# Optimization experiments

Measured on AMD Instinct MI355X. Metric: run time of the kernel, lower is better.

## Reference

```python
import jax, jax.numpy as jnp
from jax import lax
import numpy as np

VOCAB, EMB, UNITS, B, T = 32000, 256, 1024, 64, 128


def setup_inputs() -> dict:
    key = jax.random.key(0)
    k1, k2, k3, k4 = jax.random.split(key, 4)
    x = jax.random.randint(k1, (B, T), 0, VOCAB, dtype=jnp.int32)
    hidden = jnp.zeros((B, UNITS), jnp.float32)
    E = jax.random.normal(k2, (VOCAB, EMB), jnp.float32) * 0.05
    # Keras GRU kernel layout: columns = [z | r | h], each block of size UNITS
    W = jax.random.normal(k3, (EMB, 3 * UNITS), jnp.float32) * (1.0 / np.sqrt(EMB))
    U = jax.random.normal(k4, (UNITS, 3 * UNITS), jnp.float32) * (1.0 / np.sqrt(UNITS))
    b = jnp.zeros((2, 3 * UNITS), jnp.float32)  # [input_bias, recurrent_bias] (reset_after=True)
    return {"x": x, "hidden": hidden, "E": E, "W": W, "U": U, "b": b}


def reference(x, hidden, E, W, U, b):
    # Embedding lookup: [B, T, EMB]
    emb = E[x]
    # Precompute all input projections once (time-parallel GEMM): [B, T, 3*UNITS]
    xin = jnp.einsum('btd,dk->btk', emb, W) + b[0]

    def step(h, xt):
        # Recurrent projection with separate recurrent bias (reset_after=True)
        rec = h @ U + b[1]  # [B, 3*UNITS]
        xz, xr, xh = jnp.split(xt, 3, axis=-1)
        rz, rr, rh = jnp.split(rec, 3, axis=-1)
        z = jax.nn.sigmoid(xz + rz)
        r = jax.nn.sigmoid(xr + rr)
        hh = jnp.tanh(xh + r * rh)  # reset gate applied AFTER recurrent matmul
        h_new = z * h + (1.0 - z) * hh
        return h_new, h_new

    state, outs = lax.scan(step, hidden, jnp.swapaxes(xin, 0, 1))  # scan over T
    outputs = jnp.swapaxes(outs, 0, 1)  # [B, T, UNITS]
    return outputs, state
```

## Files before the change

kernel.cpp:

```cpp
#include <hip/hip_runtime.h>
#include <math.h>

typedef unsigned short u16;
typedef _Float16 f16;
typedef f16 v8h __attribute__((ext_vector_type(8)));
typedef float v4f __attribute__((ext_vector_type(4)));
typedef unsigned v4u __attribute__((ext_vector_type(4)));

union Frag { v8h h; u16 s[8]; unsigned u[4]; v4u u4; };
union HU { f16 h; u16 u; };

__device__ __forceinline__ void fsplit16s(float v, u16& hi, u16& lo) {
    HU a, b;
    float vs = v * 64.f;
    a.h = (f16)vs;
    float d = vs - (float)a.h;
    b.h = (f16)(d * 2048.f);
    hi = a.u; lo = b.u;
}

__device__ __forceinline__ void fsplit16d(double v, u16& hi, u16& lo) {
    HU a, b;
    double vs = v * 64.0;
    a.h = (f16)vs;
    float d = (float)(vs - (double)a.h);
    b.h = (f16)(d * 2048.f);
    hi = a.u; lo = b.u;
}

__device__ __forceinline__ void split8s(const float* __restrict__ p, v8h& hi, v8h& lo) {
    Frag h, l;
#pragma unroll
    for (int j = 0; j < 8; ++j) {
        u16 a, b;
        fsplit16s(p[j], a, b);
        h.s[j] = a;
        l.s[j] = b;
    }
    hi = h.h; lo = l.h;
}

__device__ __forceinline__ Frag load16_sc(const u16* p) {
    v4u r;
    asm volatile("global_load_dwordx4 %0, %1, off sc0 sc1" : "=v"(r) : "v"(p) : "memory");
    Frag f; f.u4 = r;
    return f;
}

__device__ __forceinline__ Frag load16_nc(const u16* p) {
    v4u r;
    asm volatile("global_load_dwordx4 %0, %1, off" : "=v"(r) : "v"(p) : "memory");
    Frag f; f.u4 = r;
    return f;
}

__global__ void prep_h(const float* __restrict__ hid, u16* __restrict__ hhi, u16* __restrict__ hlo) {
    int i = blockIdx.x * 256 + threadIdx.x;
    u16 h, l;
    fsplit16s(hid[i], h, l);
    hhi[i] = h;
    hlo[i] = l;
}

__global__ void transpose_split(const float* __restrict__ src, u16* __restrict__ dhi,
                                u16* __restrict__ dlo, int R, int C) {
    __shared__ float tile[32][33];
    int tid = threadIdx.x;
    int tx = tid & 31, ty = tid >> 5;
    int c0 = blockIdx.x * 32, r0 = blockIdx.y * 32;
#pragma unroll
    for (int i = 0; i < 4; ++i)
        tile[ty + i * 8][tx] = src[(size_t)(r0 + ty + i * 8) * C + c0 + tx];
    __syncthreads();
#pragma unroll
    for (int i = 0; i < 4; ++i) {
        int c = c0 + ty + i * 8;
        float v = tile[tx][ty + i * 8];
        size_t o = (size_t)c * R + r0 + tx;
        u16 h, l;
        fsplit16s(v, h, l);
        dhi[o] = h;
        dlo[o] = l;
    }
}

__global__ void init_barrier(unsigned* __restrict__ bar) {
    bar[blockIdx.x * 256 + threadIdx.x] = 0u;
}

__global__ __launch_bounds__(512, 1) void gru_persistent(
        const u16* __restrict__ UThi, const u16* __restrict__ UTlo,
        const u16* __restrict__ WThi, const u16* __restrict__ WTlo,
        const float* __restrict__ b, const int* __restrict__ x,
        const float* __restrict__ E, const float* __restrict__ hid,
        u16* __restrict__ hhi0, u16* __restrict__ hhi1,
        u16* __restrict__ hlo0, u16* __restrict__ hlo1,
        float* __restrict__ out, unsigned* __restrict__ bar) {
    __shared__ u16 u_lds[3 * 128 * 17 * 8];
    __shared__ float red[4][8][256];
    int tid = threadIdx.x;
    int w = tid >> 6, lane = tid & 63;
    int n = lane & 15, q = lane >> 4;
    int bg = blockIdx.x >> 6;
    int ut = blockIdx.x & 63;
    int b0r = bg * 16;
    int u0 = ut * 16;
    unsigned* sf = bar + bg * 256;
    unsigned* poll_addr = sf + w * 32 + (lane & 31);

    for (int i = tid; i < 3 * 128 * 16; i += 512) {
        int g = i >> 11;
        int rem = i & 2047;
        int chunk = rem >> 4;
        int col = rem & 15;
        *(v4u*)(u_lds + (size_t)((g * 128 + chunk) * 17 + col) * 8) =
            *(const v4u*)(UThi + (size_t)(g * 1024 + u0 + col) * 1024 + chunk * 8);
    }
    __syncthreads();

    size_t aoff = (size_t)(b0r + n) * 1024 + w * 128 + q * 8;
    size_t uloff = (size_t)(u0 + n) * 1024 + w * 128 + q * 8;

    Frag Wh_r[3], Wl_r[3];
#pragma unroll
    for (int g = 0; g < 3; ++g) {
        size_t wo = (size_t)(g * 1024 + u0 + n) * 256 + w * 32 + q * 8;
        Wh_r[g].u4 = *(const v4u*)(WThi + wo);
        Wl_r[g].u4 = *(const v4u*)(WTlo + wo);
    }

    const int* xrow = x + (size_t)(b0r + n) * 128;

    int bl = tid >> 4, ul = tid & 15;
    int bb = b0r + bl;
    int u = u0 + ul;
    size_t ho = (size_t)bb * 1024 + u;
    double bz = 0.0, br_ = 0.0, bxh = 0.0, brh = 0.0, hp = 0.0;
    if (tid < 256) {
        bz = (double)b[u0 + ul] + (double)b[3072 + u0 + ul];
        br_ = (double)b[1024 + u0 + ul] + (double)b[3072 + 1024 + u0 + ul];
        bxh = (double)b[2048 + u0 + ul];
        brh = (double)b[3072 + 2048 + u0 + ul];
        hp = (double)hid[ho];
    }

    const float S12 = 2.44140625e-4f;
    const float S23 = 1.1920928955078125e-7f;

    for (int t = 0; t < 128; ++t) {
        const u16* hhi_in = (t & 1) ? hhi1 : hhi0;
        const u16* hlo_in = (t & 1) ? hlo1 : hlo0;
        u16* hhi_out = (t & 1) ? hhi0 : hhi1;
        u16* hlo_out = (t & 1) ? hlo0 : hlo1;

        Frag Blo[3][4];
#pragma unroll
        for (int g = 0; g < 3; ++g)
#pragma unroll
            for (int kk = 0; kk < 4; ++kk)
                Blo[g][kk] = load16_nc(UTlo + uloff + (size_t)g * 1048576 + kk * 32);

        v4f az = {0.f, 0.f, 0.f, 0.f}, ag = az, ah = az;
        v4f azl = az, agl = az, ahl = az;
        v4f axh = az, axhl = az;

        {
            int tok = xrow[t];
            const float* erow = E + (size_t)tok * 256 + w * 32 + q * 8;
            v8h EAh, EAl;
            split8s(erow, EAh, EAl);
            az  = __builtin_amdgcn_mfma_f32_16x16x32_f16(EAh, Wh_r[0].h, az, 0, 0, 0);
            ag  = __builtin_amdgcn_mfma_f32_16x16x32_f16(EAh, Wh_r[1].h, ag, 0, 0, 0);
            axh = __builtin_amdgcn_mfma_f32_16x16x32_f16(EAh, Wh_r[2].h, axh, 0, 0, 0);
            azl  = __builtin_amdgcn_mfma_f32_16x16x32_f16(EAl, Wh_r[0].h, azl, 0, 0, 0);
            agl  = __builtin_amdgcn_mfma_f32_16x16x32_f16(EAl, Wh_r[1].h, agl, 0, 0, 0);
            axhl = __builtin_amdgcn_mfma_f32_16x16x32_f16(EAl, Wh_r[2].h, axhl, 0, 0, 0);
            azl  = __builtin_amdgcn_mfma_f32_16x16x32_f16(EAh, Wl_r[0].h, azl, 0, 0, 0);
            agl  = __builtin_amdgcn_mfma_f32_16x16x32_f16(EAh, Wl_r[1].h, agl, 0, 0, 0);
            axhl = __builtin_amdgcn_mfma_f32_16x16x32_f16(EAh, Wl_r[2].h, axhl, 0, 0, 0);
        }

        if (t > 0) {
            unsigned target = (unsigned)t;
            while (true) {
                unsigned v = __hip_atomic_load(poll_addr, __ATOMIC_RELAXED, __HIP_MEMORY_SCOPE_AGENT);
                if (__all(v >= target)) break;
                __builtin_amdgcn_s_sleep(1);
            }
        }

        v8h Ah[4], Al[4];
#pragma unroll
        for (int kk = 0; kk < 4; ++kk) {
            Ah[kk] = load16_sc(hhi_in + aoff + kk * 32).h;
            Al[kk] = load16_sc(hlo_in + aoff + kk * 32).h;
        }
        asm volatile("s_waitcnt vmcnt(0)" ::: "memory");

#pragma unroll
        for (int kk = 0; kk < 4; ++kk) {
            int chunk = w * 16 + kk * 4 + q;
            const u16* lp = u_lds + (size_t)(chunk * 17 + n) * 8;
            Frag f0, f1, f2;
            f0.u4 = *(const v4u*)(lp);
            f1.u4 = *(const v4u*)(lp + 128 * 17 * 8);
            f2.u4 = *(const v4u*)(lp + 2 * 128 * 17 * 8);
            v8h Bh0 = f0.h, Bh1 = f1.h, Bh2 = f2.h;
            az = __builtin_amdgcn_mfma_f32_16x16x32_f16(Ah[kk], Bh0, az, 0, 0, 0);
            ag = __builtin_amdgcn_mfma_f32_16x16x32_f16(Ah[kk], Bh1, ag, 0, 0, 0);
            ah = __builtin_amdgcn_mfma_f32_16x16x32_f16(Ah[kk], Bh2, ah, 0, 0, 0);
            azl = __builtin_amdgcn_mfma_f32_16x16x32_f16(Al[kk], Bh0, azl, 0, 0, 0);
            agl = __builtin_amdgcn_mfma_f32_16x16x32_f16(Al[kk], Bh1, agl, 0, 0, 0);
            ahl = __builtin_amdgcn_mfma_f32_16x16x32_f16(Al[kk], Bh2, ahl, 0, 0, 0);
            azl = __builtin_amdgcn_mfma_f32_16x16x32_f16(Ah[kk], Blo[0][kk].h, azl, 0, 0, 0);
            agl = __builtin_amdgcn_mfma_f32_16x16x32_f16(Ah[kk], Blo[1][kk].h, agl, 0, 0, 0);
            ahl = __builtin_amdgcn_mfma_f32_16x16x32_f16(Ah[kk], Blo[2][kk].h, ahl, 0, 0, 0);
        }

        __syncthreads();
#pragma unroll
        for (int r = 0; r < 4; ++r) {
            int idx = (q * 4 + r) * 16 + n;
            red[0][w][idx] = az[r] * S12 + azl[r] * S23;
            red[1][w][idx] = ag[r] * S12 + agl[r] * S23;
            red[2][w][idx] = ah[r] * S12 + ahl[r] * S23;
            red[3][w][idx] = axh[r] * S12 + axhl[r] * S23;
        }
        __syncthreads();

        if (tid < 256) {
            double rz = bz, rr = br_, rh = brh, xh = bxh;
#pragma unroll
            for (int ww = 0; ww < 8; ++ww) {
                rz += (double)red[0][ww][tid];
                rr += (double)red[1][ww][tid];
                rh += (double)red[2][ww][tid];
                xh += (double)red[3][ww][tid];
            }
            size_t bt = (size_t)bb * 128 + t;
            double z = 1.0 / (1.0 + exp(-rz));
            double rg = 1.0 / (1.0 + exp(-rr));
            double hh = tanh(xh + rg * rh);
            double hn = z * hp + (1.0 - z) * hh;
            hp = hn;
            float hnf = (float)hn;

            if (t < 127) {
                u16 myhi, mylo;
                fsplit16d(hn, myhi, mylo);
                unsigned me = (unsigned)myhi | ((unsigned)mylo << 16);
                unsigned ot = __shfl_xor(me, 1);
                if ((tid & 1) == 0) {
                    unsigned hi32 = (me & 0xFFFFu) | ((ot & 0xFFFFu) << 16);
                    unsigned lo32 = (me >> 16) | (ot & 0xFFFF0000u);
                    __hip_atomic_store((unsigned*)(hhi_out + ho), hi32, __ATOMIC_RELAXED, __HIP_MEMORY_SCOPE_AGENT);
                    __hip_atomic_store((unsigned*)(hlo_out + ho), lo32, __ATOMIC_RELAXED, __HIP_MEMORY_SCOPE_AGENT);
                }
                asm volatile("s_waitcnt vmcnt(0)" ::: "memory");
                if (lane == 0)
                    __hip_atomic_store(sf + ut * 4 + w, (unsigned)(t + 1),
                                       __ATOMIC_RELAXED, __HIP_MEMORY_SCOPE_AGENT);
            }

            __builtin_nontemporal_store(hnf, &out[bt * 1024 + u]);
            if (t == 127) __builtin_nontemporal_store(hnf, &out[8388608 + ho]);
        }
    }
}

extern "C" void kernel_launch(void* const* d_in, const int* in_sizes, int n_in,
                              void* d_out, int out_size, void* d_ws, size_t ws_size,
                              hipStream_t stream) {
    const int* x = (const int*)d_in[0];
    const float* hid = (const float*)d_in[1];
    const float* E = (const float*)d_in[2];
    const float* W = (const float*)d_in[3];
    const float* U = (const float*)d_in[4];
    const float* b = (const float*)d_in[5];
    float* out = (float*)d_out;

    char* ws = (char*)d_ws;
    u16* hhi0 = (u16*)(ws + 0);
    u16* hhi1 = (u16*)(ws + 131072);
    u16* hlo0 = (u16*)(ws + 262144);
    u16* hlo1 = (u16*)(ws + 393216);
    u16* UThi = (u16*)(ws + 524288);
    u16* UTlo = (u16*)(ws + 6815744);
    u16* WThi = (u16*)(ws + 13107200);
    u16* WTlo = (u16*)(ws + 14680064);
    unsigned* bar = (unsigned*)(ws + 16252928);

    prep_h<<<256, 256, 0, stream>>>(hid, hhi0, hlo0);
    transpose_split<<<dim3(96, 32), 256, 0, stream>>>(U, UThi, UTlo, 1024, 3072);
    transpose_split<<<dim3(96, 8), 256, 0, stream>>>(W, WThi, WTlo, 256, 3072);
    init_barrier<<<4, 256, 0, stream>>>(bar);
    gru_persistent<<<256, 512, 0, stream>>>(UThi, UTlo, WThi, WTlo, b, x, E, hid,
                                            hhi0, hhi1, hlo0, hlo1, out, bar);
}
```

Baseline: 958.4 us.

## Fuse weight transpose/split and initial hidden split into persistent GRU kernel

Removes the separate prep_h and transpose_split launches. The persistent kernel now reads fp32 U and W directly, splits them into hi/lo fp16 in its prologue, writes hi parts to LDS or registers, and writes the U lo part to workspace for later use. At t=0 it splits the fp32 initial hidden state on the fly instead of reading a prepared buffer. This saves kernel launches and a full pass over U, at the cost of strided, uncoalesced fp32 loads of U and W in the prologue.

```diff
diff --git a/kernel.cpp b/kernel.cpp
--- a/kernel.cpp
+++ b/kernel.cpp
@@ -54,43 +54,13 @@
     return f;
 }
 
-__global__ void prep_h(const float* __restrict__ hid, u16* __restrict__ hhi, u16* __restrict__ hlo) {
-    int i = blockIdx.x * 256 + threadIdx.x;
-    u16 h, l;
-    fsplit16s(hid[i], h, l);
-    hhi[i] = h;
-    hlo[i] = l;
-}
-
-__global__ void transpose_split(const float* __restrict__ src, u16* __restrict__ dhi,
-                                u16* __restrict__ dlo, int R, int C) {
-    __shared__ float tile[32][33];
-    int tid = threadIdx.x;
-    int tx = tid & 31, ty = tid >> 5;
-    int c0 = blockIdx.x * 32, r0 = blockIdx.y * 32;
-#pragma unroll
-    for (int i = 0; i < 4; ++i)
-        tile[ty + i * 8][tx] = src[(size_t)(r0 + ty + i * 8) * C + c0 + tx];
-    __syncthreads();
-#pragma unroll
-    for (int i = 0; i < 4; ++i) {
-        int c = c0 + ty + i * 8;
-        float v = tile[tx][ty + i * 8];
-        size_t o = (size_t)c * R + r0 + tx;
-        u16 h, l;
-        fsplit16s(v, h, l);
-        dhi[o] = h;
-        dlo[o] = l;
-    }
-}
-
 __global__ void init_barrier(unsigned* __restrict__ bar) {
     bar[blockIdx.x * 256 + threadIdx.x] = 0u;
 }
 
 __global__ __launch_bounds__(512, 1) void gru_persistent(
-        const u16* __restrict__ UThi, const u16* __restrict__ UTlo,
-        const u16* __restrict__ WThi, const u16* __restrict__ WTlo,
+        const float* __restrict__ U, const float* __restrict__ W,
+        u16* __restrict__ UTlo,
         const float* __restrict__ b, const int* __restrict__ x,
         const float* __restrict__ E, const float* __restrict__ hid,
         u16* __restrict__ hhi0, u16* __restrict__ hhi1,
@@ -113,9 +83,19 @@
         int rem = i & 2047;
         int chunk = rem >> 4;
         int col = rem & 15;
-        *(v4u*)(u_lds + (size_t)((g * 128 + chunk) * 17 + col) * 8) =
-            *(const v4u*)(UThi + (size_t)(g * 1024 + u0 + col) * 1024 + chunk * 8);
-    }
+        int gc = g * 1024 + u0 + col;
+        Frag h_, l_;
+#pragma unroll
+        for (int j = 0; j < 8; ++j) {
+            u16 a, bq;
+            fsplit16s(U[(size_t)(chunk * 8 + j) * 3072 + gc], a, bq);
+            h_.s[j] = a;
+            l_.s[j] = bq;
+        }
+        *(v4u*)(u_lds + (size_t)((g * 128 + chunk) * 17 + col) * 8) = h_.u4;
+        *(v4u*)(UTlo + (size_t)gc * 1024 + chunk * 8) = l_.u4;
+    }
+    asm volatile("s_waitcnt vmcnt(0)" ::: "memory");
     __syncthreads();
 
     size_t aoff = (size_t)(b0r + n) * 1024 + w * 128 + q * 8;
@@ -124,9 +104,14 @@
     Frag Wh_r[3], Wl_r[3];
 #pragma unroll
     for (int g = 0; g < 3; ++g) {
-        size_t wo = (size_t)(g * 1024 + u0 + n) * 256 + w * 32 + q * 8;
-        Wh_r[g].u4 = *(const v4u*)(WThi + wo);
-        Wl_r[g].u4 = *(const v4u*)(WTlo + wo);
+        int gc = g * 1024 + u0 + n;
+#pragma unroll
+        for (int j = 0; j < 8; ++j) {
+            u16 a, bq;
+            fsplit16s(W[(size_t)(w * 32 + q * 8 + j) * 3072 + gc], a, bq);
+            Wh_r[g].s[j] = a;
+            Wl_r[g].s[j] = bq;
+        }
     }
 
     const int* xrow = x + (size_t)(b0r + n) * 128;
@@ -180,22 +165,25 @@
             axhl = __builtin_amdgcn_mfma_f32_16x16x32_f16(EAh, Wl_r[2].h, axhl, 0, 0, 0);
         }
 
-        if (t > 0) {
+        v8h Ah[4], Al[4];
+        if (t == 0) {
+#pragma unroll
+            for (int kk = 0; kk < 4; ++kk)
+                split8s(hid + aoff + kk * 32, Ah[kk], Al[kk]);
+        } else {
             unsigned target = (unsigned)t;
             while (true) {
                 unsigned v = __hip_atomic_load(poll_addr, __ATOMIC_RELAXED, __HIP_MEMORY_SCOPE_AGENT);
                 if (__all(v >= target)) break;
                 __builtin_amdgcn_s_sleep(1);
             }
-        }
-
-        v8h Ah[4], Al[4];
-#pragma unroll
-        for (int kk = 0; kk < 4; ++kk) {
-            Ah[kk] = load16_sc(hhi_in + aoff + kk * 32).h;
-            Al[kk] = load16_sc(hlo_in + aoff + kk * 32).h;
-        }
-        asm volatile("s_waitcnt vmcnt(0)" ::: "memory");
+#pragma unroll
+            for (int kk = 0; kk < 4; ++kk) {
+                Ah[kk] = load16_sc(hhi_in + aoff + kk * 32).h;
+                Al[kk] = load16_sc(hlo_in + aoff + kk * 32).h;
+            }
+            asm volatile("s_waitcnt vmcnt(0)" ::: "memory");
+        }
 
 #pragma unroll
         for (int kk = 0; kk < 4; ++kk) {
@@ -284,16 +272,10 @@
     u16* hhi1 = (u16*)(ws + 131072);
     u16* hlo0 = (u16*)(ws + 262144);
     u16* hlo1 = (u16*)(ws + 393216);
-    u16* UThi = (u16*)(ws + 524288);
-    u16* UTlo = (u16*)(ws + 6815744);
-    u16* WThi = (u16*)(ws + 13107200);
-    u16* WTlo = (u16*)(ws + 14680064);
-    unsigned* bar = (unsigned*)(ws + 16252928);
-
-    prep_h<<<256, 256, 0, stream>>>(hid, hhi0, hlo0);
-    transpose_split<<<dim3(96, 32), 256, 0, stream>>>(U, UThi, UTlo, 1024, 3072);
-    transpose_split<<<dim3(96, 8), 256, 0, stream>>>(W, WThi, WTlo, 256, 3072);
+    u16* UTlo = (u16*)(ws + 524288);
+    unsigned* bar = (unsigned*)(ws + 6815744);
+
     init_barrier<<<4, 256, 0, stream>>>(bar);
-    gru_persistent<<<256, 512, 0, stream>>>(UThi, UTlo, WThi, WTlo, b, x, E, hid,
+    gru_persistent<<<256, 512, 0, stream>>>(U, W, UTlo, b, x, E, hid,
                                             hhi0, hhi1, hlo0, hlo1, out, bar);
 }
```

After: 944.2 us. No clear change (-1.5%).
